# Performance work log

Measured on AMD Instinct MI355X. Metric: run time of the kernel, lower is better.

## Reference

```python
import jax, jax.numpy as jnp
import numpy as np

C = 512; HEADS = 4; HD = C // HEADS
WS = (5, 9); EXP = (2, 4); FW = (5, 9)
SCALE = HD ** -0.5
B, T, NH, NW = 1, 5, 60, 108

def _valid_ind_rolled():
    wh, ww = WS; eh, ew = EXP
    tl = np.ones((wh, ww)); tl[:-eh, :-ew] = 0
    tr = np.ones((wh, ww)); tr[:-eh, ew:] = 0
    bl = np.ones((wh, ww)); bl[eh:, :-ew] = 0
    br = np.ones((wh, ww)); br[eh:, ew:] = 0
    return np.nonzero(np.stack([tl, tr, bl, br], 0).reshape(-1))[0]

VIR = jnp.asarray(_valid_ind_rolled())  # 120 valid rolled positions

def window_partition(x):
    b, t, h, w, c = x.shape
    x = x.reshape(b, t, h // WS[0], WS[0], w // WS[1], WS[1], c)
    return x.transpose(0, 2, 4, 1, 3, 5, 6).reshape(-1, t * WS[0] * WS[1], c)

def unfold(x, ker, pad):
    # torch.nn.Unfold(kernel=ker, stride=1, padding=pad): (n,c,h,w)->(n,c*kh*kw,L)
    n, c, h, w = x.shape
    xp = jnp.pad(x, ((0, 0), (0, 0), (pad[0], pad[0]), (pad[1], pad[1])))
    oh = h + 2 * pad[0] - ker[0] + 1
    ow = w + 2 * pad[1] - ker[1] + 1
    rows = jnp.arange(oh)[:, None] + jnp.arange(ker[0])[None, :]
    cols = jnp.arange(ow)[:, None] + jnp.arange(ker[1])[None, :]
    p = xp[:, :, rows[:, None, :, None], cols[None, :, None, :]]  # (n,c,oh,ow,kh,kw)
    return p.transpose(0, 1, 4, 5, 2, 3).reshape(n, c * ker[0] * ker[1], oh * ow)

def setup_inputs():
    key = jax.random.key(0)
    ks = jax.random.split(key, 4)
    return {
        "x0": jax.random.normal(ks[0], (B, T, NH, NW, C), jnp.float32),
        "x1": jax.random.normal(ks[1], (B, NH // WS[0], NW // WS[1], T, C), jnp.float32),
        "W_qkv": jax.random.normal(ks[2], (C, 3 * C), jnp.float32) * 0.02,
        "b_qkv": jnp.zeros((3 * C,), jnp.float32),
        "W_proj": jax.random.normal(ks[3], (C, C), jnp.float32) * 0.02,
        "b_proj": jnp.zeros((C,), jnp.float32),
    }

def reference(x0, x1, W_qkv, b_qkv, W_proj, b_proj):
    b, t, nh, nw, c = x0.shape
    wa = t * WS[0] * WS[1]  # tokens per window (225)
    qkv = (x0 @ W_qkv + b_qkv).reshape(b, t, nh, nw, 3, c)
    q, k, v = qkv[..., 0, :], qkv[..., 1, :], qkv[..., 2, :]

    def to_win(z):
        w = window_partition(z).reshape(-1, t, WS[0] * WS[1], HEADS, HD)
        return w.transpose(0, 3, 1, 2, 4).reshape(-1, HEADS, wa, HD)

    q_w, k_w, v_w = to_win(q), to_win(k), to_win(v)

    shifts = [(-EXP[0], -EXP[1]), (-EXP[0], EXP[1]), (EXP[0], -EXP[1]), (EXP[0], EXP[1])]
    def rolled(z):
        parts = [window_partition(jnp.roll(z, s, axis=(2, 3))).reshape(-1, t, WS[0] * WS[1], HEADS, HD) for s in shifts]
        r = jnp.concatenate(parts, axis=2).transpose(0, 3, 1, 2, 4)[:, :, :, VIR]
        return r.reshape(-1, HEADS, t * VIR.shape[0], HD)

    k_rolled = jnp.concatenate([k_w, rolled(k)], 2)
    v_rolled = jnp.concatenate([v_w, rolled(v)], 2)

    # focal level 1 pooling (focal_level=2 -> single unfold level, stride 1)
    xp = x1.transpose(0, 3, 1, 2, 4)  # (B,T,nWh,nWw,C)
    nwh, nww = xp.shape[2], xp.shape[3]
    ker = (2 * (FW[0] // 2) + 1, 2 * (FW[1] // 2) + 1)  # (5,9)
    pad = (ker[0] // 2, ker[1] // 2)
    L = nwh * nww; kk = ker[0] * ker[1]
    um = unfold(jnp.ones((t, 1, nwh, nww), x0.dtype), ker, pad)  # (T,kk,L)
    um = um.reshape(1, t, ker[0], ker[1], L).transpose(4, 1, 2, 3, 0).reshape(L, t * kk)
    pool_mask = jnp.where(um == 0, jnp.float32(-100.0), jnp.float32(0.0))  # (L, T*kk)

    qkv_p = (xp @ W_qkv + b_qkv).reshape(b, t, nwh, nww, 3, c).transpose(4, 0, 1, 5, 2, 3).reshape(3, b * t, c, nwh, nww)
    def pooled(z):
        u = unfold(z, ker, pad).reshape(b, t, c, ker[0], ker[1], L).transpose(0, 5, 1, 3, 4, 2)
        u = u.reshape(-1, t, kk, HEADS, HD).transpose(0, 3, 1, 2, 4)
        return u.reshape(-1, HEADS, t * kk, HD)

    k_all = jnp.concatenate([k_rolled, pooled(qkv_p[1])], 2)
    v_all = jnp.concatenate([v_rolled, pooled(qkv_p[2])], 2)

    attn = jnp.einsum('bhqd,bhkd->bhqk', q_w * SCALE, k_all)
    offset = k_rolled.shape[2]
    pm = jnp.tile(pool_mask[None], (b, 1, 1)).reshape(-1, t * kk)[:, None, None, :]
    attn = attn.at[:, :, :, offset:].add(pm)
    attn = jax.nn.softmax(attn, axis=-1)
    out = jnp.einsum('bhqk,bhkd->bqhd', attn, v_all).reshape(attn.shape[0], wa, c)
    return out @ W_proj + b_proj
```

## Files before the change

### kernel.cpp

```cpp
#include <hip/hip_runtime.h>

typedef _Float16 h16;
typedef __attribute__((ext_vector_type(8))) _Float16 half8;
typedef __attribute__((ext_vector_type(4))) _Float16 half4;
typedef __attribute__((ext_vector_type(2))) _Float16 half2v;
typedef __attribute__((ext_vector_type(4))) float float4v;

#define NTOK  32400
#define NPTOK 720
#define CDIM  512
#define SCALE 0.08838834764831845f
#define ZROW  NTOK
#define PROW  (NTOK + 1)

__constant__ int VIR_TBL[120] = {
  5,6,7,8, 14,15,16,17, 23,24,25,26,
  27,28,29,30,31,32,33,34,35, 36,37,38,39,40,41,42,43,44,
  45,46,47,48, 54,55,56,57, 63,64,65,66,
  72,73,74,75,76,77,78,79,80, 81,82,83,84,85,86,87,88,89,
  90,91,92,93,94,95,96,97,98, 99,100,101,102,103,104,105,106,107,
  113,114,115,116, 122,123,124,125, 131,132,133,134,
  135,136,137,138,139,140,141,142,143, 144,145,146,147,148,149,150,151,152,
  153,154,155,156, 162,163,164,165, 171,172,173,174
};

__global__ __launch_bounds__(256) void build_tok(int* __restrict__ Tok,
                                                 int* __restrict__ WMask) {
  const int win = blockIdx.x;
  const int wy = win / 12, wx = win % 12;
  for (int kidx = threadIdx.x; kidx < 1056; kidx += 256) {
    int e;
    if (kidx < 225) {
      int t = kidx / 45, pos = kidx % 45;
      int y = wy * 5 + pos / 9, x = wx * 9 + pos % 9;
      e = (t * 60 + y) * 108 + x;
    } else if (kidx < 825) {
      int jj = kidx - 225;
      int t = jj / 120, m = jj % 120;
      int vir = VIR_TBL[m];
      int p = vir / 45, pos = vir % 45;
      int r = pos / 9, c = pos % 9;
      int sy = (p < 2) ? -2 : 2;
      int sx = (p & 1) ? 4 : -4;
      int y = (wy * 5 + r - sy + 60) % 60;
      int x = (wx * 9 + c - sx + 108) % 108;
      e = (t * 60 + y) * 108 + x;
    } else if (kidx < 1050) {
      int jp = kidx - 825;
      int t = jp / 45, pos = jp % 45;
      int py = wy + pos / 9 - 2;
      int px = wx + pos % 9 - 4;
      e = (py >= 0 && py < 12 && px >= 0 && px < 12)
            ? (PROW + t * 144 + py * 12 + px) : ZROW;
    } else {
      e = ZROW;
    }
    Tok[win * 1056 + kidx] = e;
  }
  if (threadIdx.x < 33) {
    int m = 0;
#pragma unroll 1
    for (int r = 0; r < 32; r++) {
      int kidx = threadIdx.x * 32 + r;
      bool v;
      if (kidx < 825) v = true;
      else if (kidx < 1050) {
        int jp = kidx - 825, pos = jp % 45;
        int py = wy + pos / 9 - 2, px = wx + pos % 9 - 4;
        v = (py >= 0 && py < 12 && px >= 0 && px < 12);
      } else v = false;
      m |= (v ? 1 : 0) << r;
    }
    WMask[win * 33 + threadIdx.x] = m;
  }
}

__global__ __launch_bounds__(256) void zero_rows(h16* __restrict__ a,
                                                 h16* __restrict__ b) {
  for (int k = threadIdx.x; k < 512; k += 256) {
    a[(size_t)ZROW * CDIM + k] = (h16)0.f;
    b[(size_t)ZROW * CDIM + k] = (h16)0.f;
  }
}

__global__ __launch_bounds__(256) void transpose_cvt(const float* __restrict__ src,
                                                     h16* __restrict__ dst,
                                                     int R, int C) {
  __shared__ float T[32][33];
  const int t = threadIdx.x;
  const int ct = blockIdx.x * 32;
  const int rt = blockIdx.y * 32;
  const int c = t & 31, r0 = (t >> 5) * 4;
#pragma unroll
  for (int i = 0; i < 4; i++)
    T[r0 + i][c] = src[(size_t)(rt + r0 + i) * C + ct + c];
  __syncthreads();
#pragma unroll
  for (int i = 0; i < 4; i++)
    dst[(size_t)(ct + r0 + i) * R + rt + c] = (h16)T[c][r0 + i];
}

struct StageLDS { h16 Ah[128][40]; h16 Bh[128][40]; };
union GemmLDS { StageLDS s; h16 Cs[128][136]; };

__global__ __launch_bounds__(256) void gemm_qkv_mfma(
    const float* __restrict__ A, const h16* __restrict__ Bt,
    const float* __restrict__ bias,
    h16* __restrict__ Q, h16* __restrict__ K, h16* __restrict__ V)
{
  __shared__ GemmLDS u;
  const int tid = threadIdx.x;
  const int lane = tid & 63, wv = tid >> 6;
  const int col = lane & 15, quad = lane >> 4;
  const int bm = blockIdx.x, bn = blockIdx.y;
  const int mo = (wv & 1) * 64, no = (wv >> 1) * 64;

  float4v acc[4][4];
#pragma unroll
  for (int i = 0; i < 4; i++)
#pragma unroll
    for (int j = 0; j < 4; j++) acc[i][j] = (float4v){0.f, 0.f, 0.f, 0.f};

  const int srow = tid >> 1, skoff = (tid & 1) * 16;
  const int arow = bm * 128 + srow;
  const float* Ap = A + (size_t)arow * 512 + skoff;
  const h16* Bp = Bt + (size_t)(bn * 128 + srow) * 512 + skoff;

  for (int k0 = 0; k0 < 512; k0 += 32) {
    half8 a0, a1, b0, b1;
    if (arow < NTOK) {
      float4 f0 = *(const float4*)(Ap + k0);
      float4 f1 = *(const float4*)(Ap + k0 + 4);
      float4 f2 = *(const float4*)(Ap + k0 + 8);
      float4 f3 = *(const float4*)(Ap + k0 + 12);
      a0[0]=(h16)f0.x; a0[1]=(h16)f0.y; a0[2]=(h16)f0.z; a0[3]=(h16)f0.w;
      a0[4]=(h16)f1.x; a0[5]=(h16)f1.y; a0[6]=(h16)f1.z; a0[7]=(h16)f1.w;
      a1[0]=(h16)f2.x; a1[1]=(h16)f2.y; a1[2]=(h16)f2.z; a1[3]=(h16)f2.w;
      a1[4]=(h16)f3.x; a1[5]=(h16)f3.y; a1[6]=(h16)f3.z; a1[7]=(h16)f3.w;
    } else {
#pragma unroll
      for (int jj = 0; jj < 8; jj++) { a0[jj] = (h16)0.f; a1[jj] = (h16)0.f; }
    }
    b0 = *(const half8*)(Bp + k0);
    b1 = *(const half8*)(Bp + k0 + 8);
    __syncthreads();
    *(half8*)&u.s.Ah[srow][skoff] = a0;
    *(half8*)&u.s.Ah[srow][skoff + 8] = a1;
    *(half8*)&u.s.Bh[srow][skoff] = b0;
    *(half8*)&u.s.Bh[srow][skoff + 8] = b1;
    __syncthreads();

    half8 afr[4], bfr[4];
#pragma unroll
    for (int i = 0; i < 4; i++)
      afr[i] = *(const half8*)&u.s.Ah[mo + i * 16 + col][quad * 8];
#pragma unroll
    for (int j = 0; j < 4; j++)
      bfr[j] = *(const half8*)&u.s.Bh[no + j * 16 + col][quad * 8];
#pragma unroll
    for (int i = 0; i < 4; i++)
#pragma unroll
      for (int j = 0; j < 4; j++)
        acc[i][j] = __builtin_amdgcn_mfma_f32_16x16x32_f16(afr[i], bfr[j], acc[i][j], 0, 0, 0);
  }

  __syncthreads();
  float bv[4];
#pragma unroll
  for (int j = 0; j < 4; j++) bv[j] = bias[bn * 128 + no + j * 16 + col];
#pragma unroll
  for (int i = 0; i < 4; i++)
#pragma unroll
    for (int j = 0; j < 4; j++)
#pragma unroll
      for (int r = 0; r < 4; r++)
        u.Cs[mo + i * 16 + quad * 4 + r][no + j * 16 + col] = (h16)(acc[i][j][r] + bv[j]);
  __syncthreads();

  const int row_l = tid >> 1, halfseg = (tid & 1) * 64;
  const int row_g = bm * 128 + row_l;
  const int jsel = bn >> 2;
  const int ch0 = (bn & 3) * 128 + halfseg;
  h16* dst = (jsel == 0) ? Q : (jsel == 1) ? K : V;
  if (row_g < NTOK) {
#pragma unroll
    for (int c = 0; c < 64; c += 8)
      *(half8*)&dst[(size_t)row_g * 512 + ch0 + c] = *(const half8*)&u.Cs[row_l][halfseg + c];
  }
}

__global__ __launch_bounds__(256) void gemm_proj_mfma(
    const h16* __restrict__ A, const h16* __restrict__ Bt,
    const float* __restrict__ bias, float* __restrict__ out)
{
  __shared__ StageLDS s;
  const int tid = threadIdx.x;
  const int lane = tid & 63, wv = tid >> 6;
  const int col = lane & 15, quad = lane >> 4;
  const int bm = blockIdx.x, bn = blockIdx.y;
  const int mo = (wv & 1) * 64, no = (wv >> 1) * 64;

  float4v acc[4][4];
#pragma unroll
  for (int i = 0; i < 4; i++)
#pragma unroll
    for (int j = 0; j < 4; j++) acc[i][j] = (float4v){0.f, 0.f, 0.f, 0.f};

  const int srow = tid >> 1, skoff = (tid & 1) * 16;
  const int arow = bm * 128 + srow;
  const h16* Ap = A + (size_t)arow * 512 + skoff;
  const h16* Bp = Bt + (size_t)(bn * 128 + srow) * 512 + skoff;

  for (int k0 = 0; k0 < 512; k0 += 32) {
    half8 a0, a1, b0, b1;
    if (arow < NTOK) {
      a0 = *(const half8*)(Ap + k0);
      a1 = *(const half8*)(Ap + k0 + 8);
    } else {
#pragma unroll
      for (int jj = 0; jj < 8; jj++) { a0[jj] = (h16)0.f; a1[jj] = (h16)0.f; }
    }
    b0 = *(const half8*)(Bp + k0);
    b1 = *(const half8*)(Bp + k0 + 8);
    __syncthreads();
    *(half8*)&s.Ah[srow][skoff] = a0;
    *(half8*)&s.Ah[srow][skoff + 8] = a1;
    *(half8*)&s.Bh[srow][skoff] = b0;
    *(half8*)&s.Bh[srow][skoff + 8] = b1;
    __syncthreads();

    half8 afr[4], bfr[4];
#pragma unroll
    for (int i = 0; i < 4; i++)
      afr[i] = *(const half8*)&s.Ah[mo + i * 16 + col][quad * 8];
#pragma unroll
    for (int j = 0; j < 4; j++)
      bfr[j] = *(const half8*)&s.Bh[no + j * 16 + col][quad * 8];
#pragma unroll
    for (int i = 0; i < 4; i++)
#pragma unroll
      for (int j = 0; j < 4; j++)
        acc[i][j] = __builtin_amdgcn_mfma_f32_16x16x32_f16(afr[i], bfr[j], acc[i][j], 0, 0, 0);
  }

  float bv[4];
#pragma unroll
  for (int j = 0; j < 4; j++) bv[j] = bias[bn * 128 + no + j * 16 + col];
#pragma unroll
  for (int i = 0; i < 4; i++) {
#pragma unroll
    for (int r = 0; r < 4; r++) {
      int row_g = bm * 128 + mo + i * 16 + quad * 4 + r;
      if (row_g < NTOK) {
#pragma unroll
        for (int j = 0; j < 4; j++)
          out[(size_t)row_g * 512 + bn * 128 + no + j * 16 + col] = acc[i][j][r] + bv[j];
      }
    }
  }
}

__global__ __launch_bounds__(256) void gemm_pooled(
    const float* __restrict__ A, const float* __restrict__ B,
    const float* __restrict__ bias,
    h16* __restrict__ Kp, h16* __restrict__ Vp)
{
  __shared__ float As[64][17];
  __shared__ float Bs[16][64];
  const int tid = threadIdx.x;
  const int bm = blockIdx.x, bn = blockIdx.y;
  const int tm = tid >> 4, tn = tid & 15;
  const int lrow = tid >> 2, lk = (tid & 3) * 4;
  const int brow = tid >> 4, bcol = (tid & 15) * 4;
  float acc[4][4] = {};
  const int orow = bm * 64 + lrow;
  int srow = 0;
  if (orow < NPTOK) { int t = orow / 144, rem = orow % 144; srow = rem * 5 + t; }
  const float* Ap = A + (size_t)srow * 512 + lk;
  const float* Bp = B + (size_t)brow * 1536 + 512 + bn * 64 + bcol;

  for (int k0 = 0; k0 < 512; k0 += 16) {
    float4 av = make_float4(0.f, 0.f, 0.f, 0.f);
    if (orow < NPTOK) av = *(const float4*)(Ap + k0);
    float4 bv = *(const float4*)(Bp + (size_t)k0 * 1536);
    As[lrow][lk + 0] = av.x; As[lrow][lk + 1] = av.y;
    As[lrow][lk + 2] = av.z; As[lrow][lk + 3] = av.w;
    *(float4*)&Bs[brow][bcol] = bv;
    __syncthreads();
#pragma unroll
    for (int kk = 0; kk < 16; kk++) {
      float a[4];
#pragma unroll
      for (int i = 0; i < 4; i++) a[i] = As[tm * 4 + i][kk];
      float4 b = *(const float4*)&Bs[kk][tn * 4];
#pragma unroll
      for (int i = 0; i < 4; i++) {
        acc[i][0] = fmaf(a[i], b.x, acc[i][0]);
        acc[i][1] = fmaf(a[i], b.y, acc[i][1]);
        acc[i][2] = fmaf(a[i], b.z, acc[i][2]);
        acc[i][3] = fmaf(a[i], b.w, acc[i][3]);
      }
    }
    __syncthreads();
  }
  const int nl = bn * 64 + tn * 4;
  const int j = nl >> 9;
  const int ch = nl & 511;
  h16* dst = (j == 0) ? Kp : Vp;
#pragma unroll
  for (int i = 0; i < 4; i++) {
    int r = bm * 64 + tm * 4 + i;
    if (r < NPTOK) {
#pragma unroll
      for (int c = 0; c < 4; c++)
        dst[(size_t)r * 512 + ch + c] = (h16)(acc[i][c] + bias[512 + nl + c]);
    }
  }
}

__global__ __launch_bounds__(256, 3) void attn_kernel(
    const h16* __restrict__ Qh, const h16* __restrict__ KhU,
    const h16* __restrict__ VhU, const int* __restrict__ Tok,
    const int* __restrict__ WMask, h16* __restrict__ AOh)
{
  __shared__ h16 Ks[32 * 136];
  __shared__ h16 Vt[128 * 40];

  const int tid = threadIdx.x;
  const int lane = tid & 63;
  const int wv = tid >> 6;
  const int win = blockIdx.x;
  const int head = blockIdx.y;
  const int qg = blockIdx.z;
  const int wy = win / 12, wx = win % 12;
  const int col = lane & 15;
  const int quad = lane >> 4;
  const int* TokW = Tok + win * 1056;
  const int* WMaskW = WMask + win * 33;

  half8 qfrag[2][4];
  const int tile0 = qg * 8 + wv * 2;
#pragma unroll
  for (int tt = 0; tt < 2; tt++) {
    int qrow = (tile0 + tt) * 16 + col;
    if (qrow < 225) {
      int t = qrow / 45, pos = qrow % 45;
      int y = wy * 5 + pos / 9, x = wx * 9 + pos % 9;
      const h16* qsrc = Qh + (size_t)((t * 60 + y) * 108 + x) * CDIM + head * 128;
#pragma unroll
      for (int dc = 0; dc < 4; dc++)
        qfrag[tt][dc] = *(const half8*)(qsrc + dc * 32 + quad * 8);
    } else {
#pragma unroll
      for (int dc = 0; dc < 4; dc++)
#pragma unroll
        for (int jj = 0; jj < 8; jj++) qfrag[tt][dc][jj] = (h16)0.f;
    }
  }

  float4v O[2][8];
#pragma unroll
  for (int tt = 0; tt < 2; tt++)
#pragma unroll
    for (int i = 0; i < 8; i++) O[tt][i] = (float4v){0.f, 0.f, 0.f, 0.f};
  float lp[2] = {0.f, 0.f};

  const int krow = tid >> 3, kseg = tid & 7;
  const int vrp = tid >> 4, vcg = tid & 15;
  const int kch = head * 128 + kseg * 16;
  const int vch = head * 128 + vcg * 8;
  const int vrot = (vcg & 3) * 4;
  const int rp = (vrp + vrot) & 15;

  int tokK[2], tokVa[2], tokVb[2];
  tokK[0]  = TokW[krow];          tokK[1]  = TokW[32 + krow];
  tokVa[0] = TokW[2 * vrp];       tokVa[1] = TokW[32 + 2 * vrp];
  tokVb[0] = TokW[2 * vrp + 1];   tokVb[1] = TokW[32 + 2 * vrp + 1];
  half8 k0c, k1c, vac, vbc, k0n, k1n, van, vbn;
  {
    const h16* ks = KhU + (size_t)tokK[0] * CDIM + kch;
    k0c = *(const half8*)ks;
    k1c = *(const half8*)(ks + 8);
    vac = *(const half8*)(VhU + (size_t)tokVa[0] * CDIM + vch);
    vbc = *(const half8*)(VhU + (size_t)tokVb[0] * CDIM + vch);
  }

  for (int step = 0; step < 33; ++step) {
    __syncthreads();
    *(half8*)&Ks[krow * 136 + kseg * 16] = k0c;
    *(half8*)&Ks[krow * 136 + kseg * 16 + 8] = k1c;
#pragma unroll
    for (int i = 0; i < 8; i++) {
      half2v w; w[0] = vac[i]; w[1] = vbc[i];
      *(half2v*)&Vt[(vcg * 8 + i) * 40 + rp * 2] = w;
    }
    if (step + 1 < 33) {
      const h16* ks = KhU + (size_t)tokK[(step + 1) & 1] * CDIM + kch;
      k0n = *(const half8*)ks;
      k1n = *(const half8*)(ks + 8);
      van = *(const half8*)(VhU + (size_t)tokVa[(step + 1) & 1] * CDIM + vch);
      vbn = *(const half8*)(VhU + (size_t)tokVb[(step + 1) & 1] * CDIM + vch);
      if (step + 2 < 33) {
        tokK[step & 1]  = TokW[(step + 2) * 32 + krow];
        tokVa[step & 1] = TokW[(step + 2) * 32 + 2 * vrp];
        tokVb[step & 1] = TokW[(step + 2) * 32 + 2 * vrp + 1];
      }
    }
    __syncthreads();

    const int mask = WMaskW[step];

    float4v s0[2] = {{0.f,0.f,0.f,0.f},{0.f,0.f,0.f,0.f}};
    float4v s1[2] = {{0.f,0.f,0.f,0.f},{0.f,0.f,0.f,0.f}};
#pragma unroll
    for (int dc = 0; dc < 4; dc++) {
      half8 a0 = *(const half8*)&Ks[col * 136 + dc * 32 + quad * 8];
      half8 a1 = *(const half8*)&Ks[(col + 16) * 136 + dc * 32 + quad * 8];
#pragma unroll
      for (int tt = 0; tt < 2; tt++) {
        s0[tt] = __builtin_amdgcn_mfma_f32_16x16x32_f16(a0, qfrag[tt][dc], s0[tt], 0, 0, 0);
        s1[tt] = __builtin_amdgcn_mfma_f32_16x16x32_f16(a1, qfrag[tt][dc], s1[tt], 0, 0, 0);
      }
    }

    half8 pfrag[2];
    const int srcA = (((quad << 1) & 3) << 4) | col;
    const int srcB = ((((quad << 1) + 1) & 3) << 4) | col;
    const bool hi = quad >= 2;
#pragma unroll
    for (int tt = 0; tt < 2; tt++) {
      float pm0[4], pm1[4];
#pragma unroll
      for (int i = 0; i < 4; i++) {
        int r = quad * 4 + i;
        float e0 = __expf(s0[tt][i] * SCALE);
        float e1 = __expf(s1[tt][i] * SCALE);
        pm0[i] = ((mask >> r) & 1) ? e0 : 0.f;
        pm1[i] = ((mask >> (16 + r)) & 1) ? e1 : 0.f;
        lp[tt] += pm0[i] + pm1[i];
      }
      float g00 = __builtin_bit_cast(float, __builtin_amdgcn_cvt_pkrtz(pm0[0], pm0[1]));
      float g01 = __builtin_bit_cast(float, __builtin_amdgcn_cvt_pkrtz(pm0[2], pm0[3]));
      float g10 = __builtin_bit_cast(float, __builtin_amdgcn_cvt_pkrtz(pm1[0], pm1[1]));
      float g11 = __builtin_bit_cast(float, __builtin_amdgcn_cvt_pkrtz(pm1[2], pm1[3]));
      float a0 = __shfl(g00, srcA), a1 = __shfl(g01, srcA);
      float a2 = __shfl(g00, srcB), a3 = __shfl(g01, srcB);
      float b0 = __shfl(g10, srcA), b1 = __shfl(g11, srcA);
      float b2 = __shfl(g10, srcB), b3 = __shfl(g11, srcB);
      float4v pf;
      pf[0] = hi ? b0 : a0;
      pf[1] = hi ? b1 : a1;
      pf[2] = hi ? b2 : a2;
      pf[3] = hi ? b3 : a3;
      pfrag[tt] = __builtin_bit_cast(half8, pf);
    }

#pragma unroll
    for (int dt = 0; dt < 8; dt++) {
      int ch = dt * 16 + col;
      int g4 = ((dt * 2 + (col >> 3)) & 3) * 4;
      int x0 = (quad * 4 + g4) & 15;
      half8 vf = *(const half8*)&Vt[ch * 40 + x0 * 2];
#pragma unroll
      for (int tt = 0; tt < 2; tt++)
        O[tt][dt] = __builtin_amdgcn_mfma_f32_16x16x32_f16(pfrag[tt], vf, O[tt][dt], 0, 0, 0);
    }

    k0c = k0n; k1c = k1n; vac = van; vbc = vbn;
  }

#pragma unroll
  for (int tt = 0; tt < 2; tt++) {
    float l_all = lp[tt];
    l_all += __shfl_xor(l_all, 16);
    l_all += __shfl_xor(l_all, 32);
#pragma unroll
    for (int i = 0; i < 4; i++) {
      int qr = (tile0 + tt) * 16 + quad * 4 + i;
      if (qr < 225) {
        float invl = __builtin_amdgcn_rcpf(__shfl(l_all, quad * 4 + i));
        h16* dst = AOh + ((size_t)win * 225 + qr) * CDIM + head * 128 + col;
#pragma unroll
        for (int dt = 0; dt < 8; dt++)
          dst[dt * 16] = (h16)(O[tt][dt][i] * invl);
      }
    }
  }
}

extern "C" void kernel_launch(void* const* d_in, const int* in_sizes, int n_in,
                              void* d_out, int out_size, void* d_ws, size_t ws_size,
                              hipStream_t stream) {
  const float* x0    = (const float*)d_in[0];
  const float* x1    = (const float*)d_in[1];
  const float* Wqkv  = (const float*)d_in[2];
  const float* bqkv  = (const float*)d_in[3];
  const float* Wproj = (const float*)d_in[4];
  const float* bproj = (const float*)d_in[5];
  float* out = (float*)d_out;

  const size_t NU = (size_t)(NTOK + 1 + NPTOK);
  h16* Qh   = (h16*)d_ws;
  h16* KhU  = Qh + (size_t)NTOK * CDIM;
  h16* VhU  = KhU + NU * CDIM;
  h16* AOh  = VhU + NU * CDIM;
  h16* Wqkvt  = AOh + (size_t)NTOK * CDIM;
  h16* Wprojt = Wqkvt + (size_t)1536 * 512;
  int* Tok    = (int*)(Wprojt + (size_t)512 * 512);
  int* WMaskP = Tok + (size_t)144 * 1056;

  build_tok<<<144, 256, 0, stream>>>(Tok, WMaskP);
  zero_rows<<<1, 256, 0, stream>>>(KhU, VhU);
  transpose_cvt<<<dim3(48, 16), 256, 0, stream>>>(Wqkv, Wqkvt, 512, 1536);
  transpose_cvt<<<dim3(16, 16), 256, 0, stream>>>(Wproj, Wprojt, 512, 512);

  gemm_qkv_mfma<<<dim3(254, 12), 256, 0, stream>>>(x0, Wqkvt, bqkv, Qh, KhU, VhU);
  gemm_pooled<<<dim3(12, 16), 256, 0, stream>>>(x1, Wqkv, bqkv,
                                                KhU + (size_t)PROW * CDIM,
                                                VhU + (size_t)PROW * CDIM);
  attn_kernel<<<dim3(144, 4, 2), 256, 0, stream>>>(Qh, KhU, VhU, Tok, WMaskP, AOh);
  gemm_proj_mfma<<<dim3(254, 4), 256, 0, stream>>>(AOh, Wprojt, bproj, out);
}
```

Baseline: 513.4 us.

## Use direct global-to-LDS loads in GEMMs, pre-convert x0, double-buffer attention K/V

Adds a separate kernel that converts x0 to fp16 once, so the QKV GEMM reads fp16 activations. Both MFMA GEMMs now stage their tiles with global_load_lds straight into unpadded LDS and swap grid axes so blocks sharing an M tile run together. The attention kernel double-buffers K/V in LDS with one barrier per step, prefetches two steps ahead, raises launch bounds to 4 waves and sets wave priority around MFMA sections. The trade-offs are an extra conversion pass over x0, possible LDS bank conflicts from the unpadded 32-wide rows, and more LDS use in attention, which could limit occupancy.

```diff
diff --git a/kernel.cpp b/kernel.cpp
--- a/kernel.cpp
+++ b/kernel.cpp
@@ -2,9 +2,11 @@
 
 typedef _Float16 h16;
 typedef __attribute__((ext_vector_type(8))) _Float16 half8;
-typedef __attribute__((ext_vector_type(4))) _Float16 half4;
 typedef __attribute__((ext_vector_type(2))) _Float16 half2v;
 typedef __attribute__((ext_vector_type(4))) float float4v;
+
+typedef const __attribute__((address_space(1))) unsigned char gu8;
+typedef __attribute__((address_space(3))) unsigned char su8;
 
 #define NTOK  32400
 #define NPTOK 720
@@ -100,11 +102,24 @@
     dst[(size_t)(ct + r0 + i) * R + rt + c] = (h16)T[c][r0 + i];
 }
 
-struct StageLDS { h16 Ah[128][40]; h16 Bh[128][40]; };
-union GemmLDS { StageLDS s; h16 Cs[128][136]; };
+__global__ __launch_bounds__(256) void cvt_x0(const float* __restrict__ src,
+                                              h16* __restrict__ dst) {
+  const int total = NTOK * CDIM / 8;
+  for (int i = blockIdx.x * 256 + threadIdx.x; i < total; i += gridDim.x * 256) {
+    const float4* s = (const float4*)(src + (size_t)i * 8);
+    float4 f0 = s[0], f1 = s[1];
+    half8 h;
+    h[0] = (h16)f0.x; h[1] = (h16)f0.y; h[2] = (h16)f0.z; h[3] = (h16)f0.w;
+    h[4] = (h16)f1.x; h[5] = (h16)f1.y; h[6] = (h16)f1.z; h[7] = (h16)f1.w;
+    *(half8*)(dst + (size_t)i * 8) = h;
+  }
+}
+
+struct __align__(16) StageLDS { h16 Ah[128][32]; h16 Bh[128][32]; };
+union __align__(16) GemmLDS { StageLDS s; h16 Cs[128][136]; };
 
 __global__ __launch_bounds__(256) void gemm_qkv_mfma(
-    const float* __restrict__ A, const h16* __restrict__ Bt,
+    const h16* __restrict__ A, const h16* __restrict__ Bt,
     const float* __restrict__ bias,
     h16* __restrict__ Q, h16* __restrict__ K, h16* __restrict__ V)
 {
@@ -112,7 +127,7 @@
   const int tid = threadIdx.x;
   const int lane = tid & 63, wv = tid >> 6;
   const int col = lane & 15, quad = lane >> 4;
-  const int bm = blockIdx.x, bn = blockIdx.y;
+  const int bn = blockIdx.x, bm = blockIdx.y;
   const int mo = (wv & 1) * 64, no = (wv >> 1) * 64;
 
   float4v acc[4][4];
@@ -121,33 +136,22 @@
 #pragma unroll
     for (int j = 0; j < 4; j++) acc[i][j] = (float4v){0.f, 0.f, 0.f, 0.f};
 
-  const int srow = tid >> 1, skoff = (tid & 1) * 16;
-  const int arow = bm * 128 + srow;
-  const float* Ap = A + (size_t)arow * 512 + skoff;
-  const h16* Bp = Bt + (size_t)(bn * 128 + srow) * 512 + skoff;
+  const int lrow = lane >> 2, lcol = (lane & 3) * 8;
+  const int arow = bm * 128 + wv * 32 + lrow;
+  const int ar = arow < NTOK ? arow : (NTOK - 1);
+  const int ar2 = (arow + 16) < NTOK ? (arow + 16) : (NTOK - 1);
+  const h16* Ag  = A + (size_t)ar * 512 + lcol;
+  const h16* Ag2 = A + (size_t)ar2 * 512 + lcol;
+  const h16* Bg  = Bt + (size_t)(bn * 128 + wv * 32 + lrow) * 512 + lcol;
+  su8* Al = (su8*)&u.s.Ah[wv * 32][0];
+  su8* Bl = (su8*)&u.s.Bh[wv * 32][0];
 
   for (int k0 = 0; k0 < 512; k0 += 32) {
-    half8 a0, a1, b0, b1;
-    if (arow < NTOK) {
-      float4 f0 = *(const float4*)(Ap + k0);
-      float4 f1 = *(const float4*)(Ap + k0 + 4);
-      float4 f2 = *(const float4*)(Ap + k0 + 8);
-      float4 f3 = *(const float4*)(Ap + k0 + 12);
-      a0[0]=(h16)f0.x; a0[1]=(h16)f0.y; a0[2]=(h16)f0.z; a0[3]=(h16)f0.w;
-      a0[4]=(h16)f1.x; a0[5]=(h16)f1.y; a0[6]=(h16)f1.z; a0[7]=(h16)f1.w;
-      a1[0]=(h16)f2.x; a1[1]=(h16)f2.y; a1[2]=(h16)f2.z; a1[3]=(h16)f2.w;
-      a1[4]=(h16)f3.x; a1[5]=(h16)f3.y; a1[6]=(h16)f3.z; a1[7]=(h16)f3.w;
-    } else {
-#pragma unroll
-      for (int jj = 0; jj < 8; jj++) { a0[jj] = (h16)0.f; a1[jj] = (h16)0.f; }
-    }
-    b0 = *(const half8*)(Bp + k0);
-    b1 = *(const half8*)(Bp + k0 + 8);
-    __syncthreads();
-    *(half8*)&u.s.Ah[srow][skoff] = a0;
-    *(half8*)&u.s.Ah[srow][skoff + 8] = a1;
-    *(half8*)&u.s.Bh[srow][skoff] = b0;
-    *(half8*)&u.s.Bh[srow][skoff + 8] = b1;
+    __syncthreads();
+    __builtin_amdgcn_global_load_lds((gu8*)(Ag + k0),            Al,        16, 0, 0);
+    __builtin_amdgcn_global_load_lds((gu8*)(Ag2 + k0),           Al + 1024, 16, 0, 0);
+    __builtin_amdgcn_global_load_lds((gu8*)(Bg + k0),            Bl,        16, 0, 0);
+    __builtin_amdgcn_global_load_lds((gu8*)(Bg + k0 + 16 * 512), Bl + 1024, 16, 0, 0);
     __syncthreads();
 
     half8 afr[4], bfr[4];
@@ -197,7 +201,7 @@
   const int tid = threadIdx.x;
   const int lane = tid & 63, wv = tid >> 6;
   const int col = lane & 15, quad = lane >> 4;
-  const int bm = blockIdx.x, bn = blockIdx.y;
+  const int bn = blockIdx.x, bm = blockIdx.y;
   const int mo = (wv & 1) * 64, no = (wv >> 1) * 64;
 
   float4v acc[4][4];
@@ -206,27 +210,22 @@
 #pragma unroll
     for (int j = 0; j < 4; j++) acc[i][j] = (float4v){0.f, 0.f, 0.f, 0.f};
 
-  const int srow = tid >> 1, skoff = (tid & 1) * 16;
-  const int arow = bm * 128 + srow;
-  const h16* Ap = A + (size_t)arow * 512 + skoff;
-  const h16* Bp = Bt + (size_t)(bn * 128 + srow) * 512 + skoff;
+  const int lrow = lane >> 2, lcol = (lane & 3) * 8;
+  const int arow = bm * 128 + wv * 32 + lrow;
+  const int ar = arow < NTOK ? arow : (NTOK - 1);
+  const int ar2 = (arow + 16) < NTOK ? (arow + 16) : (NTOK - 1);
+  const h16* Ag  = A + (size_t)ar * 512 + lcol;
+  const h16* Ag2 = A + (size_t)ar2 * 512 + lcol;
+  const h16* Bg  = Bt + (size_t)(bn * 128 + wv * 32 + lrow) * 512 + lcol;
+  su8* Al = (su8*)&s.Ah[wv * 32][0];
+  su8* Bl = (su8*)&s.Bh[wv * 32][0];
 
   for (int k0 = 0; k0 < 512; k0 += 32) {
-    half8 a0, a1, b0, b1;
-    if (arow < NTOK) {
-      a0 = *(const half8*)(Ap + k0);
-      a1 = *(const half8*)(Ap + k0 + 8);
-    } else {
-#pragma unroll
-      for (int jj = 0; jj < 8; jj++) { a0[jj] = (h16)0.f; a1[jj] = (h16)0.f; }
-    }
-    b0 = *(const half8*)(Bp + k0);
-    b1 = *(const half8*)(Bp + k0 + 8);
-    __syncthreads();
-    *(half8*)&s.Ah[srow][skoff] = a0;
-    *(half8*)&s.Ah[srow][skoff + 8] = a1;
-    *(half8*)&s.Bh[srow][skoff] = b0;
-    *(half8*)&s.Bh[srow][skoff + 8] = b1;
+    __syncthreads();
+    __builtin_amdgcn_global_load_lds((gu8*)(Ag + k0),            Al,        16, 0, 0);
+    __builtin_amdgcn_global_load_lds((gu8*)(Ag2 + k0),           Al + 1024, 16, 0, 0);
+    __builtin_amdgcn_global_load_lds((gu8*)(Bg + k0),            Bl,        16, 0, 0);
+    __builtin_amdgcn_global_load_lds((gu8*)(Bg + k0 + 16 * 512), Bl + 1024, 16, 0, 0);
     __syncthreads();
 
     half8 afr[4], bfr[4];
@@ -318,13 +317,13 @@
   }
 }
 
-__global__ __launch_bounds__(256, 3) void attn_kernel(
+__global__ __launch_bounds__(256, 4) void attn_kernel(
     const h16* __restrict__ Qh, const h16* __restrict__ KhU,
     const h16* __restrict__ VhU, const int* __restrict__ Tok,
     const int* __restrict__ WMask, h16* __restrict__ AOh)
 {
-  __shared__ h16 Ks[32 * 136];
-  __shared__ h16 Vt[128 * 40];
+  __shared__ __align__(16) h16 Ks[2][32 * 136];
+  __shared__ __align__(16) h16 Vt[2][128 * 40];
 
   const int tid = threadIdx.x;
   const int lane = tid & 63;
@@ -369,59 +368,80 @@
   const int vrp = tid >> 4, vcg = tid & 15;
   const int kch = head * 128 + kseg * 16;
   const int vch = head * 128 + vcg * 8;
-  const int vrot = (vcg & 3) * 4;
-  const int rp = (vrp + vrot) & 15;
-
-  int tokK[2], tokVa[2], tokVb[2];
-  tokK[0]  = TokW[krow];          tokK[1]  = TokW[32 + krow];
-  tokVa[0] = TokW[2 * vrp];       tokVa[1] = TokW[32 + 2 * vrp];
-  tokVb[0] = TokW[2 * vrp + 1];   tokVb[1] = TokW[32 + 2 * vrp + 1];
-  half8 k0c, k1c, vac, vbc, k0n, k1n, van, vbn;
+  const int rp = (vrp + (vcg & 3) * 4) & 15;
+
   {
-    const h16* ks = KhU + (size_t)tokK[0] * CDIM + kch;
-    k0c = *(const half8*)ks;
-    k1c = *(const half8*)(ks + 8);
-    vac = *(const half8*)(VhU + (size_t)tokVa[0] * CDIM + vch);
-    vbc = *(const half8*)(VhU + (size_t)tokVb[0] * CDIM + vch);
-  }
-
-  for (int step = 0; step < 33; ++step) {
-    __syncthreads();
-    *(half8*)&Ks[krow * 136 + kseg * 16] = k0c;
-    *(half8*)&Ks[krow * 136 + kseg * 16 + 8] = k1c;
+    const h16* ks = KhU + (size_t)TokW[krow] * CDIM + kch;
+    half8 k0c = *(const half8*)ks;
+    half8 k1c = *(const half8*)(ks + 8);
+    half8 vac = *(const half8*)(VhU + (size_t)TokW[2 * vrp] * CDIM + vch);
+    half8 vbc = *(const half8*)(VhU + (size_t)TokW[2 * vrp + 1] * CDIM + vch);
+    *(half8*)&Ks[0][krow * 136 + kseg * 16] = k0c;
+    *(half8*)&Ks[0][krow * 136 + kseg * 16 + 8] = k1c;
 #pragma unroll
     for (int i = 0; i < 8; i++) {
       half2v w; w[0] = vac[i]; w[1] = vbc[i];
-      *(half2v*)&Vt[(vcg * 8 + i) * 40 + rp * 2] = w;
-    }
+      *(half2v*)&Vt[0][(vcg * 8 + i) * 40 + rp * 2] = w;
+    }
+  }
+  half8 k0n, k1n, van, vbn;
+  {
+    const h16* ks = KhU + (size_t)TokW[32 + krow] * CDIM + kch;
+    k0n = *(const half8*)ks;
+    k1n = *(const half8*)(ks + 8);
+    van = *(const half8*)(VhU + (size_t)TokW[32 + 2 * vrp] * CDIM + vch);
+    vbn = *(const half8*)(VhU + (size_t)TokW[32 + 2 * vrp + 1] * CDIM + vch);
+  }
+  int tokK[2], tokVa[2], tokVb[2];
+  tokK[0] = TokW[64 + krow]; tokVa[0] = TokW[64 + 2 * vrp]; tokVb[0] = TokW[64 + 2 * vrp + 1];
+  tokK[1] = TokW[96 + krow]; tokVa[1] = TokW[96 + 2 * vrp]; tokVb[1] = TokW[96 + 2 * vrp + 1];
+  __syncthreads();
+
+  for (int step = 0; step < 33; ++step) {
+    const int cur = step & 1;
+
     if (step + 1 < 33) {
-      const h16* ks = KhU + (size_t)tokK[(step + 1) & 1] * CDIM + kch;
+      h16* KsN = Ks[cur ^ 1];
+      h16* VtN = Vt[cur ^ 1];
+      *(half8*)&KsN[krow * 136 + kseg * 16] = k0n;
+      *(half8*)&KsN[krow * 136 + kseg * 16 + 8] = k1n;
+#pragma unroll
+      for (int i = 0; i < 8; i++) {
+        half2v w; w[0] = van[i]; w[1] = vbn[i];
+        *(half2v*)&VtN[(vcg * 8 + i) * 40 + rp * 2] = w;
+      }
+    }
+    if (step + 2 < 33) {
+      const h16* ks = KhU + (size_t)tokK[cur] * CDIM + kch;
       k0n = *(const half8*)ks;
       k1n = *(const half8*)(ks + 8);
-      van = *(const half8*)(VhU + (size_t)tokVa[(step + 1) & 1] * CDIM + vch);
-      vbn = *(const half8*)(VhU + (size_t)tokVb[(step + 1) & 1] * CDIM + vch);
-      if (step + 2 < 33) {
-        tokK[step & 1]  = TokW[(step + 2) * 32 + krow];
-        tokVa[step & 1] = TokW[(step + 2) * 32 + 2 * vrp];
-        tokVb[step & 1] = TokW[(step + 2) * 32 + 2 * vrp + 1];
-      }
-    }
-    __syncthreads();
+      van = *(const half8*)(VhU + (size_t)tokVa[cur] * CDIM + vch);
+      vbn = *(const half8*)(VhU + (size_t)tokVb[cur] * CDIM + vch);
+      if (step + 4 < 33) {
+        tokK[cur]  = TokW[(step + 4) * 32 + krow];
+        tokVa[cur] = TokW[(step + 4) * 32 + 2 * vrp];
+        tokVb[cur] = TokW[(step + 4) * 32 + 2 * vrp + 1];
+      }
+    }
 
     const int mask = WMaskW[step];
+    const h16* KsC = Ks[cur];
+    const h16* VtC = Vt[cur];
 
     float4v s0[2] = {{0.f,0.f,0.f,0.f},{0.f,0.f,0.f,0.f}};
     float4v s1[2] = {{0.f,0.f,0.f,0.f},{0.f,0.f,0.f,0.f}};
+    __builtin_amdgcn_s_setprio(1);
 #pragma unroll
     for (int dc = 0; dc < 4; dc++) {
-      half8 a0 = *(const half8*)&Ks[col * 136 + dc * 32 + quad * 8];
-      half8 a1 = *(const half8*)&Ks[(col + 16) * 136 + dc * 32 + quad * 8];
+      half8 a0 = *(const half8*)&KsC[col * 136 + dc * 32 + quad * 8];
+      half8 a1 = *(const half8*)&KsC[(col + 16) * 136 + dc * 32 + quad * 8];
 #pragma unroll
       for (int tt = 0; tt < 2; tt++) {
         s0[tt] = __builtin_amdgcn_mfma_f32_16x16x32_f16(a0, qfrag[tt][dc], s0[tt], 0, 0, 0);
         s1[tt] = __builtin_amdgcn_mfma_f32_16x16x32_f16(a1, qfrag[tt][dc], s1[tt], 0, 0, 0);
       }
     }
+    __builtin_amdgcn_s_setprio(0);
 
     half8 pfrag[2];
     const int srcA = (((quad << 1) & 3) << 4) | col;
@@ -455,18 +475,20 @@
       pfrag[tt] = __builtin_bit_cast(half8, pf);
     }
 
+    __builtin_amdgcn_s_setprio(1);
 #pragma unroll
     for (int dt = 0; dt < 8; dt++) {
       int ch = dt * 16 + col;
       int g4 = ((dt * 2 + (col >> 3)) & 3) * 4;
       int x0 = (quad * 4 + g4) & 15;
-      half8 vf = *(const half8*)&Vt[ch * 40 + x0 * 2];
+      half8 vf = *(const half8*)&VtC[ch * 40 + x0 * 2];
 #pragma unroll
       for (int tt = 0; tt < 2; tt++)
         O[tt][dt] = __builtin_amdgcn_mfma_f32_16x16x32_f16(pfrag[tt], vf, O[tt][dt], 0, 0, 0);
     }
-
-    k0c = k0n; k1c = k1n; vac = van; vbc = vbn;
+    __builtin_amdgcn_s_setprio(0);
+
+    __syncthreads();
   }
 
 #pragma unroll
@@ -503,8 +525,8 @@
   h16* Qh   = (h16*)d_ws;
   h16* KhU  = Qh + (size_t)NTOK * CDIM;
   h16* VhU  = KhU + NU * CDIM;
-  h16* AOh  = VhU + NU * CDIM;
-  h16* Wqkvt  = AOh + (size_t)NTOK * CDIM;
+  h16* Rh   = VhU + NU * CDIM;
+  h16* Wqkvt  = Rh + (size_t)NTOK * CDIM;
   h16* Wprojt = Wqkvt + (size_t)1536 * 512;
   int* Tok    = (int*)(Wprojt + (size_t)512 * 512);
   int* WMaskP = Tok + (size_t)144 * 1056;
@@ -513,11 +535,12 @@
   zero_rows<<<1, 256, 0, stream>>>(KhU, VhU);
   transpose_cvt<<<dim3(48, 16), 256, 0, stream>>>(Wqkv, Wqkvt, 512, 1536);
   transpose_cvt<<<dim3(16, 16), 256, 0, stream>>>(Wproj, Wprojt, 512, 512);
-
-  gemm_qkv_mfma<<<dim3(254, 12), 256, 0, stream>>>(x0, Wqkvt, bqkv, Qh, KhU, VhU);
+  cvt_x0<<<2048, 256, 0, stream>>>(x0, Rh);
+
+  gemm_qkv_mfma<<<dim3(12, 254), 256, 0, stream>>>(Rh, Wqkvt, bqkv, Qh, KhU, VhU);
   gemm_pooled<<<dim3(12, 16), 256, 0, stream>>>(x1, Wqkv, bqkv,
                                                 KhU + (size_t)PROW * CDIM,
                                                 VhU + (size_t)PROW * CDIM);
-  attn_kernel<<<dim3(144, 4, 2), 256, 0, stream>>>(Qh, KhU, VhU, Tok, WMaskP, AOh);
-  gemm_proj_mfma<<<dim3(254, 4), 256, 0, stream>>>(AOh, Wprojt, bproj, out);
-}
+  attn_kernel<<<dim3(144, 4, 2), 256, 0, stream>>>(Qh, KhU, VhU, Tok, WMaskP, Rh);
+  gemm_proj_mfma<<<dim3(4, 254), 256, 0, stream>>>(Rh, Wprojt, bproj, out);
+}
```

Measured after the change: 758.2 us. +47.7%, slower.
